# Optimization experiments

Hardware: AMD Instinct MI355X
Metric: run time of the kernel (lower is better)

Reference implementation:

```python
import jax, jax.numpy as jnp
import numpy as np

TOTAL_N = 1_048_576
FEAT = 128
B = 8
VOX_AXIS = 40  # 40**3 = 64000 <= num_vox (65535) hard-coded in the kernel
SUBBUCK = 2    # module asserts subbuck_size == 2


def setup_inputs() -> dict:
    key = jax.random.key(0)
    k1, k2 = jax.random.split(key)
    coords = jax.random.uniform(k1, (TOTAL_N, 3), dtype=jnp.float32) * 100.0
    input_feat = jax.random.normal(k2, (TOTAL_N, FEAT), dtype=jnp.float32)
    # seps = exclusive-scan ends of each batch instance (equal-size instances)
    seps = jnp.arange(1, B + 1, dtype=jnp.int32) * (TOTAL_N // B)
    return {"coords": coords, "input_feat": input_feat, "seps": seps}


def _bucket_order(coords, seps):
    """Per-instance voxel-bucket assignment + stable sort; returns (order, unpool_ind, inst_id)."""
    n = coords.shape[0]
    nb = seps.shape[0]
    # instance id of every point from cumulative boundaries
    inst_id = jnp.searchsorted(seps, jnp.arange(n, dtype=seps.dtype), side="right").astype(jnp.int32)
    # per-instance bounding box (bbox_min / bbox_max buffers in the CUDA kernel)
    bmin = jax.ops.segment_min(coords, inst_id, num_segments=nb)
    bmax = jax.ops.segment_max(coords, inst_id, num_segments=nb)
    lo, hi = bmin[inst_id], bmax[inst_id]
    u = (coords - lo) / jnp.maximum(hi - lo, jnp.float32(1e-12))
    q = jnp.clip((u * VOX_AXIS).astype(jnp.int32), 0, VOX_AXIS - 1)  # (N,3) voxel coords
    vox_id = (q[:, 0] * VOX_AXIS + q[:, 1]) * VOX_AXIS + q[:, 2]      # subbuck_id
    # stable sort by (instance, voxel) so spatially-colocated points are adjacent
    key = inst_id.astype(jnp.int64) * (VOX_AXIS ** 3) + vox_id.astype(jnp.int64)
    order = jnp.argsort(key)  # jnp.argsort is stable
    # consecutive pairs in sorted order form one subbucket of size 2
    reduced_rank = jnp.arange(n, dtype=jnp.int32) // SUBBUCK
    unpool_ind = jnp.zeros((n,), dtype=jnp.int32).at[order].set(reduced_rank)
    return order, unpool_ind, inst_id


def reference(coords, input_feat, seps):
    n = input_feat.shape[0]
    reduced_n = n // SUBBUCK
    _, unpool_ind, _ = _bucket_order(coords, seps)
    # mean reduction (reduction_op = 0 = O_MEAN) over each subbucket of 2 points
    reduced_feat = jax.ops.segment_sum(input_feat, unpool_ind, num_segments=reduced_n) / SUBBUCK
    reduced_coord = jax.ops.segment_sum(coords, unpool_ind, num_segments=reduced_n) / SUBBUCK
    reduced_sep = seps // SUBBUCK
    return reduced_coord, reduced_sep, reduced_feat, unpool_ind
```

## Files before the change

### kernel.cpp

```cpp
#include <hip/hip_runtime.h>


#define VOXA 40
#define VOX3 64000
#define SCAN_CHUNK 2048

__device__ __forceinline__ int inst_of(int i, const int* __restrict__ seps, int B) {
  int lo = 0, hi = B;
  while (lo < hi) { int m = (lo + hi) >> 1; if (seps[m] > i) hi = m; else lo = m + 1; }
  return lo;
}

__device__ __forceinline__ unsigned fmap(float f) {
  unsigned u = __float_as_uint(f);
  return (u & 0x80000000u) ? ~u : (u | 0x80000000u);
}
__device__ __forceinline__ float funmap(unsigned u) {
  unsigned b = (u & 0x80000000u) ? (u ^ 0x80000000u) : ~u;
  return __uint_as_float(b);
}

__global__ void k_init(int* hist, int* cursor, unsigned* bbox, int K, int B3) {
  int i = blockIdx.x * blockDim.x + threadIdx.x;
  if (i < K) { hist[i] = 0; cursor[i] = 0; }
  if (i < B3) { bbox[i] = 0xFFFFFFFFu; bbox[B3 + i] = 0u; }
}

__global__ void k_bbox(const float* __restrict__ coords, const int* __restrict__ seps,
                       int N, int B, unsigned* __restrict__ bbox) {
  const int CH = 1024;
  int cs = blockIdx.x * CH;
  if (cs >= N) return;
  int ce = min(cs + CH, N);
  __shared__ int uni;
  int t = threadIdx.x;
  if (t == 0) {
    int i0 = inst_of(cs, seps, B);
    int i1 = inst_of(ce - 1, seps, B);
    uni = (i0 == i1) ? i0 : -1;
  }
  __syncthreads();
  if (uni >= 0) {
    float mn0 = 3.4e38f, mn1 = 3.4e38f, mn2 = 3.4e38f;
    float mx0 = -3.4e38f, mx1 = -3.4e38f, mx2 = -3.4e38f;
    for (int i = cs + t; i < ce; i += 256) {
      float c0 = coords[i * 3 + 0], c1 = coords[i * 3 + 1], c2 = coords[i * 3 + 2];
      mn0 = fminf(mn0, c0); mn1 = fminf(mn1, c1); mn2 = fminf(mn2, c2);
      mx0 = fmaxf(mx0, c0); mx1 = fmaxf(mx1, c1); mx2 = fmaxf(mx2, c2);
    }
    __shared__ float sm[6][256];
    sm[0][t] = mn0; sm[1][t] = mn1; sm[2][t] = mn2;
    sm[3][t] = mx0; sm[4][t] = mx1; sm[5][t] = mx2;
    __syncthreads();
    for (int s = 128; s > 0; s >>= 1) {
      if (t < s) {
        sm[0][t] = fminf(sm[0][t], sm[0][t + s]);
        sm[1][t] = fminf(sm[1][t], sm[1][t + s]);
        sm[2][t] = fminf(sm[2][t], sm[2][t + s]);
        sm[3][t] = fmaxf(sm[3][t], sm[3][t + s]);
        sm[4][t] = fmaxf(sm[4][t], sm[4][t + s]);
        sm[5][t] = fmaxf(sm[5][t], sm[5][t + s]);
      }
      __syncthreads();
    }
    if (t == 0) {
      int b = uni;
      atomicMin(&bbox[b * 3 + 0], fmap(sm[0][0]));
      atomicMin(&bbox[b * 3 + 1], fmap(sm[1][0]));
      atomicMin(&bbox[b * 3 + 2], fmap(sm[2][0]));
      atomicMax(&bbox[B * 3 + b * 3 + 0], fmap(sm[3][0]));
      atomicMax(&bbox[B * 3 + b * 3 + 1], fmap(sm[4][0]));
      atomicMax(&bbox[B * 3 + b * 3 + 2], fmap(sm[5][0]));
    }
  } else {
    for (int i = cs + t; i < ce; i += 256) {
      int b = inst_of(i, seps, B);
      for (int d = 0; d < 3; ++d) {
        float c = coords[i * 3 + d];
        atomicMin(&bbox[b * 3 + d], fmap(c));
        atomicMax(&bbox[B * 3 + b * 3 + d], fmap(c));
      }
    }
  }
}

__global__ void k_key(const float* __restrict__ coords, const int* __restrict__ seps,
                      int N, int B, const unsigned* __restrict__ bbox,
                      int* __restrict__ key, int* __restrict__ hist) {
  __shared__ float lo[192], hi[192];
  int t = threadIdx.x;
  if (t < 3 * B) { lo[t] = funmap(bbox[t]); hi[t] = funmap(bbox[3 * B + t]); }
  __syncthreads();
  int i = blockIdx.x * blockDim.x + t;
  if (i >= N) return;
  int b = inst_of(i, seps, B);
  int q[3];
#pragma unroll
  for (int d = 0; d < 3; ++d) {
    float c = coords[i * 3 + d];
    float l = lo[b * 3 + d];
    float u = (c - l) / fmaxf(hi[b * 3 + d] - l, 1e-12f);
    int qi = (int)(u * 40.0f);
    q[d] = min(max(qi, 0), VOXA - 1);
  }
  int k = ((q[0] * VOXA + q[1]) * VOXA + q[2]) + b * VOX3;
  key[i] = k;
  atomicAdd(&hist[k], 1);
}

__global__ void k_scan1(int* __restrict__ hist, int* __restrict__ csums, int K) {
  __shared__ int s[256];
  int t = threadIdx.x;
  int base = blockIdx.x * SCAN_CHUNK + t * 8;
  int v[8];
  int run = 0;
#pragma unroll
  for (int j = 0; j < 8; ++j) {
    int idx = base + j;
    int x = (idx < K) ? hist[idx] : 0;
    v[j] = run;
    run += x;
  }
  s[t] = run;
  __syncthreads();
  for (int off = 1; off < 256; off <<= 1) {
    int x = (t >= off) ? s[t - off] : 0;
    __syncthreads();
    s[t] += x;
    __syncthreads();
  }
  int excl = s[t] - run;
#pragma unroll
  for (int j = 0; j < 8; ++j) {
    int idx = base + j;
    if (idx < K) hist[idx] = excl + v[j];
  }
  if (t == 255) csums[blockIdx.x] = s[255];
}

__global__ void k_scan2(int* csums, int nChunks) {
  __shared__ int s[256];
  int t = threadIdx.x;
  int carry = 0;
  for (int base = 0; base < nChunks; base += 256) {
    int idx = base + t;
    int v = (idx < nChunks) ? csums[idx] : 0;
    s[t] = v;
    __syncthreads();
    for (int off = 1; off < 256; off <<= 1) {
      int x = (t >= off) ? s[t - off] : 0;
      __syncthreads();
      s[t] += x;
      __syncthreads();
    }
    if (idx < nChunks) csums[idx] = carry + s[t] - v;
    int total = s[255];
    __syncthreads();
    carry += total;
  }
}

__global__ void k_scan3(int* __restrict__ hist, const int* __restrict__ csums, int K) {
  int i = blockIdx.x * blockDim.x + threadIdx.x;
  if (i < K) hist[i] += csums[i / SCAN_CHUNK];
}

__global__ void k_place(const int* __restrict__ key, const int* __restrict__ start,
                        int* __restrict__ cursor, int* __restrict__ order, int N) {
  int i = blockIdx.x * blockDim.x + threadIdx.x;
  if (i >= N) return;
  int k = key[i];
  int r = atomicAdd(&cursor[k], 1);
  order[start[k] + r] = i;
}

__global__ void k_fix(const int* __restrict__ start, int* __restrict__ order, int K, int N) {
  int k = blockIdx.x * blockDim.x + threadIdx.x;
  if (k >= K) return;
  int s = start[k];
  int e = (k + 1 < K) ? start[k + 1] : N;
  for (int a = s + 1; a < e; ++a) {
    int v = order[a];
    int b = a - 1;
    while (b >= s && order[b] > v) { order[b + 1] = order[b]; --b; }
    order[b + 1] = v;
  }
}

__global__ void k_out_coord(const float* __restrict__ coords, const int* __restrict__ order,
                            const int* __restrict__ seps, int RN, int B,
                            float* __restrict__ out) {
  int r = blockIdx.x * blockDim.x + threadIdx.x;
  if (r < B) out[(size_t)RN * 3 + r] = (float)(seps[r] / 2);
  if (r >= RN) return;
  int a = order[2 * r], b = order[2 * r + 1];
  out[r * 3 + 0] = (coords[a * 3 + 0] + coords[b * 3 + 0]) * 0.5f;
  out[r * 3 + 1] = (coords[a * 3 + 1] + coords[b * 3 + 1]) * 0.5f;
  out[r * 3 + 2] = (coords[a * 3 + 2] + coords[b * 3 + 2]) * 0.5f;
}

__global__ void k_out_feat(const float4* __restrict__ feat4, const int* __restrict__ order,
                           int RN, float4* __restrict__ outf) {
  int tid = blockIdx.x * blockDim.x + threadIdx.x;
  if (tid >= RN * 32) return;
  int r = tid >> 5, c = tid & 31;
  int a = order[2 * r], b = order[2 * r + 1];
  float4 va = feat4[a * 32 + c], vb = feat4[b * 32 + c];
  float4 o;
  o.x = (va.x + vb.x) * 0.5f;
  o.y = (va.y + vb.y) * 0.5f;
  o.z = (va.z + vb.z) * 0.5f;
  o.w = (va.w + vb.w) * 0.5f;
  outf[tid] = o;
}

__global__ void k_out_feat_scalar(const float* __restrict__ feat, const int* __restrict__ order,
                                  int RN, float* __restrict__ outf) {
  int tid = blockIdx.x * blockDim.x + threadIdx.x;
  if (tid >= RN * 128) return;
  int r = tid >> 7, c = tid & 127;
  int a = order[2 * r], b = order[2 * r + 1];
  outf[tid] = (feat[a * 128 + c] + feat[b * 128 + c]) * 0.5f;
}

__global__ void k_out_unpool(const int* __restrict__ order, float* __restrict__ outu, int N) {
  int p = blockIdx.x * blockDim.x + threadIdx.x;
  if (p >= N) return;
  outu[order[p]] = (float)(p >> 1);
}

extern "C" void kernel_launch(void* const* d_in, const int* in_sizes, int n_in,
                              void* d_out, int out_size, void* d_ws, size_t ws_size,
                              hipStream_t stream) {
  const float* coords = (const float*)d_in[0];
  const float* feat   = (const float*)d_in[1];
  const int*   seps   = (const int*)d_in[2];

  const int N  = in_sizes[0] / 3;
  const int B  = in_sizes[2];
  const int FE = in_sizes[1] / N;
  const int RN = N / 2;
  const int K  = B * VOX3;
  const int nChunks = (K + SCAN_CHUNK - 1) / SCAN_CHUNK;

  int* hist      = (int*)d_ws;
  int* cursor    = hist + K;
  int* csums     = cursor + K;
  unsigned* bbox = (unsigned*)(csums + ((nChunks + 255) & ~255));
  int* key       = (int*)(bbox + 6 * B);
  int* order     = key + N;

  float* out        = (float*)d_out;
  float* out_coord  = out;
  float* out_feat   = out + (size_t)RN * 3 + B;
  float* out_unpool = out_feat + (size_t)RN * FE;

  const int blk = 256;
  k_init<<<(K + blk - 1) / blk, blk, 0, stream>>>(hist, cursor, bbox, K, 3 * B);
  k_bbox<<<(N + 1023) / 1024, 256, 0, stream>>>(coords, seps, N, B, bbox);
  k_key<<<(N + blk - 1) / blk, blk, 0, stream>>>(coords, seps, N, B, bbox, key, hist);
  k_scan1<<<nChunks, 256, 0, stream>>>(hist, csums, K);
  k_scan2<<<1, 256, 0, stream>>>(csums, nChunks);
  k_scan3<<<(K + blk - 1) / blk, blk, 0, stream>>>(hist, csums, K);
  k_place<<<(N + blk - 1) / blk, blk, 0, stream>>>(key, hist, cursor, order, N);
  k_fix<<<(K + blk - 1) / blk, blk, 0, stream>>>(hist, order, K, N);
  k_out_coord<<<(RN + blk - 1) / blk, blk, 0, stream>>>(coords, order, seps, RN, B, out_coord);

  bool vec_ok = (FE % 4 == 0) && ((((size_t)RN * 3 + B) & 3) == 0) && (FE == 128);
  if (vec_ok) {
    k_out_feat<<<((RN * 32) + blk - 1) / blk, blk, 0, stream>>>(
        (const float4*)feat, order, RN, (float4*)out_feat);
  } else {
    k_out_feat_scalar<<<((RN * FE) + blk - 1) / blk, blk, 0, stream>>>(
        feat, order, RN, out_feat);
  }
  k_out_unpool<<<(N + blk - 1) / blk, blk, 0, stream>>>(order, out_unpool, N);
}
```

Measured before the change: 939.0 us.

## Fuse scan-add into placement, unpool into fix, coord into feature gather

Removes the scan3 pass by adding the chunk offset on the fly in placement and reusing the histogram as the cursor array, which drops the separate cursor buffer and its zeroing. Unpool writes and seps output move into the per-bucket sort-fix kernel. Coordinate averaging is merged into the feature gather kernel, which now uses an int2 pair load plus nontemporal vector loads and stores. Seps are cached in shared memory for the key kernel. The trade-offs are more serial per-bucket work in the fix kernel and more complex index arithmetic.

```diff
diff --git a/kernel.cpp b/kernel.cpp
--- a/kernel.cpp
+++ b/kernel.cpp
@@ -4,6 +4,8 @@
 #define VOXA 40
 #define VOX3 64000
 #define SCAN_CHUNK 2048
+
+typedef float f4 __attribute__((ext_vector_type(4)));
 
 __device__ __forceinline__ int inst_of(int i, const int* __restrict__ seps, int B) {
   int lo = 0, hi = B;
@@ -11,6 +13,12 @@
   return lo;
 }
 
+__device__ __forceinline__ int inst_of_s(int i, const int* s, int B) {
+  int lo = 0, hi = B;
+  while (lo < hi) { int m = (lo + hi) >> 1; if (s[m] > i) hi = m; else lo = m + 1; }
+  return lo;
+}
+
 __device__ __forceinline__ unsigned fmap(float f) {
   unsigned u = __float_as_uint(f);
   return (u & 0x80000000u) ? ~u : (u | 0x80000000u);
@@ -20,9 +28,9 @@
   return __uint_as_float(b);
 }
 
-__global__ void k_init(int* hist, int* cursor, unsigned* bbox, int K, int B3) {
+__global__ void k_init(int* hist, unsigned* bbox, int K, int B3) {
   int i = blockIdx.x * blockDim.x + threadIdx.x;
-  if (i < K) { hist[i] = 0; cursor[i] = 0; }
+  if (i < K) hist[i] = 0;
   if (i < B3) { bbox[i] = 0xFFFFFFFFu; bbox[B3 + i] = 0u; }
 }
 
@@ -88,12 +96,14 @@
                       int N, int B, const unsigned* __restrict__ bbox,
                       int* __restrict__ key, int* __restrict__ hist) {
   __shared__ float lo[192], hi[192];
+  __shared__ int ssep[64];
   int t = threadIdx.x;
   if (t < 3 * B) { lo[t] = funmap(bbox[t]); hi[t] = funmap(bbox[3 * B + t]); }
+  if (t < B) ssep[t] = seps[t];
   __syncthreads();
   int i = blockIdx.x * blockDim.x + t;
   if (i >= N) return;
-  int b = inst_of(i, seps, B);
+  int b = inst_of_s(i, ssep, B);
   int q[3];
 #pragma unroll
   for (int d = 0; d < 3; ++d) {
@@ -160,73 +170,65 @@
   }
 }
 
-__global__ void k_scan3(int* __restrict__ hist, const int* __restrict__ csums, int K) {
-  int i = blockIdx.x * blockDim.x + threadIdx.x;
-  if (i < K) hist[i] += csums[i / SCAN_CHUNK];
-}
-
-__global__ void k_place(const int* __restrict__ key, const int* __restrict__ start,
-                        int* __restrict__ cursor, int* __restrict__ order, int N) {
+__global__ void k_place(const int* __restrict__ key, int* __restrict__ hist,
+                        const int* __restrict__ csums, int* __restrict__ order, int N) {
   int i = blockIdx.x * blockDim.x + threadIdx.x;
   if (i >= N) return;
   int k = key[i];
-  int r = atomicAdd(&cursor[k], 1);
-  order[start[k] + r] = i;
-}
-
-__global__ void k_fix(const int* __restrict__ start, int* __restrict__ order, int K, int N) {
+  int p = atomicAdd(&hist[k], 1) + csums[k / SCAN_CHUNK];
+  order[p] = i;
+}
+
+__global__ void k_fix(const int* __restrict__ hist, const int* __restrict__ csums,
+                      int* __restrict__ order, float* __restrict__ outu,
+                      const int* __restrict__ seps, float* __restrict__ out_sep,
+                      int K, int N, int B) {
   int k = blockIdx.x * blockDim.x + threadIdx.x;
+  if (k < B) out_sep[k] = (float)(seps[k] / 2);
   if (k >= K) return;
-  int s = start[k];
-  int e = (k + 1 < K) ? start[k + 1] : N;
+  int e = hist[k] + csums[k / SCAN_CHUNK];
+  int s = (k == 0) ? 0 : (hist[k - 1] + csums[(k - 1) / SCAN_CHUNK]);
   for (int a = s + 1; a < e; ++a) {
     int v = order[a];
     int b = a - 1;
     while (b >= s && order[b] > v) { order[b + 1] = order[b]; --b; }
     order[b + 1] = v;
   }
-}
-
-__global__ void k_out_coord(const float* __restrict__ coords, const int* __restrict__ order,
-                            const int* __restrict__ seps, int RN, int B,
-                            float* __restrict__ out) {
-  int r = blockIdx.x * blockDim.x + threadIdx.x;
-  if (r < B) out[(size_t)RN * 3 + r] = (float)(seps[r] / 2);
-  if (r >= RN) return;
-  int a = order[2 * r], b = order[2 * r + 1];
-  out[r * 3 + 0] = (coords[a * 3 + 0] + coords[b * 3 + 0]) * 0.5f;
-  out[r * 3 + 1] = (coords[a * 3 + 1] + coords[b * 3 + 1]) * 0.5f;
-  out[r * 3 + 2] = (coords[a * 3 + 2] + coords[b * 3 + 2]) * 0.5f;
-}
-
-__global__ void k_out_feat(const float4* __restrict__ feat4, const int* __restrict__ order,
-                           int RN, float4* __restrict__ outf) {
+  for (int p = s; p < e; ++p) outu[order[p]] = (float)(p >> 1);
+}
+
+__global__ void k_out_fused(const f4* __restrict__ feat4, const float* __restrict__ coords,
+                            const int* __restrict__ order, int RN,
+                            float* __restrict__ out_coord, f4* __restrict__ outf) {
   int tid = blockIdx.x * blockDim.x + threadIdx.x;
   if (tid >= RN * 32) return;
   int r = tid >> 5, c = tid & 31;
+  int2 ab = ((const int2*)order)[r];
+  int a = ab.x, b = ab.y;
+  f4 va = __builtin_nontemporal_load(&feat4[(size_t)a * 32 + c]);
+  f4 vb = __builtin_nontemporal_load(&feat4[(size_t)b * 32 + c]);
+  f4 o = (va + vb) * 0.5f;
+  __builtin_nontemporal_store(o, &outf[tid]);
+  if (c == 0) {
+    out_coord[r * 3 + 0] = (coords[a * 3 + 0] + coords[b * 3 + 0]) * 0.5f;
+    out_coord[r * 3 + 1] = (coords[a * 3 + 1] + coords[b * 3 + 1]) * 0.5f;
+    out_coord[r * 3 + 2] = (coords[a * 3 + 2] + coords[b * 3 + 2]) * 0.5f;
+  }
+}
+
+__global__ void k_out_fused_scalar(const float* __restrict__ feat, const float* __restrict__ coords,
+                                   const int* __restrict__ order, int RN, int FE,
+                                   float* __restrict__ out_coord, float* __restrict__ outf) {
+  int tid = blockIdx.x * blockDim.x + threadIdx.x;
+  if (tid >= RN * FE) return;
+  int r = tid / FE, c = tid % FE;
   int a = order[2 * r], b = order[2 * r + 1];
-  float4 va = feat4[a * 32 + c], vb = feat4[b * 32 + c];
-  float4 o;
-  o.x = (va.x + vb.x) * 0.5f;
-  o.y = (va.y + vb.y) * 0.5f;
-  o.z = (va.z + vb.z) * 0.5f;
-  o.w = (va.w + vb.w) * 0.5f;
-  outf[tid] = o;
-}
-
-__global__ void k_out_feat_scalar(const float* __restrict__ feat, const int* __restrict__ order,
-                                  int RN, float* __restrict__ outf) {
-  int tid = blockIdx.x * blockDim.x + threadIdx.x;
-  if (tid >= RN * 128) return;
-  int r = tid >> 7, c = tid & 127;
-  int a = order[2 * r], b = order[2 * r + 1];
-  outf[tid] = (feat[a * 128 + c] + feat[b * 128 + c]) * 0.5f;
-}
-
-__global__ void k_out_unpool(const int* __restrict__ order, float* __restrict__ outu, int N) {
-  int p = blockIdx.x * blockDim.x + threadIdx.x;
-  if (p >= N) return;
-  outu[order[p]] = (float)(p >> 1);
+  outf[tid] = (feat[(size_t)a * FE + c] + feat[(size_t)b * FE + c]) * 0.5f;
+  if (c == 0) {
+    out_coord[r * 3 + 0] = (coords[a * 3 + 0] + coords[b * 3 + 0]) * 0.5f;
+    out_coord[r * 3 + 1] = (coords[a * 3 + 1] + coords[b * 3 + 1]) * 0.5f;
+    out_coord[r * 3 + 2] = (coords[a * 3 + 2] + coords[b * 3 + 2]) * 0.5f;
+  }
 }
 
 extern "C" void kernel_launch(void* const* d_in, const int* in_sizes, int n_in,
@@ -244,35 +246,33 @@
   const int nChunks = (K + SCAN_CHUNK - 1) / SCAN_CHUNK;
 
   int* hist      = (int*)d_ws;
-  int* cursor    = hist + K;
-  int* csums     = cursor + K;
+  int* csums     = hist + K;
   unsigned* bbox = (unsigned*)(csums + ((nChunks + 255) & ~255));
   int* key       = (int*)(bbox + 6 * B);
   int* order     = key + N;
 
   float* out        = (float*)d_out;
   float* out_coord  = out;
+  float* out_sep    = out + (size_t)RN * 3;
   float* out_feat   = out + (size_t)RN * 3 + B;
   float* out_unpool = out_feat + (size_t)RN * FE;
 
   const int blk = 256;
-  k_init<<<(K + blk - 1) / blk, blk, 0, stream>>>(hist, cursor, bbox, K, 3 * B);
+  k_init<<<(K + blk - 1) / blk, blk, 0, stream>>>(hist, bbox, K, 3 * B);
   k_bbox<<<(N + 1023) / 1024, 256, 0, stream>>>(coords, seps, N, B, bbox);
   k_key<<<(N + blk - 1) / blk, blk, 0, stream>>>(coords, seps, N, B, bbox, key, hist);
   k_scan1<<<nChunks, 256, 0, stream>>>(hist, csums, K);
   k_scan2<<<1, 256, 0, stream>>>(csums, nChunks);
-  k_scan3<<<(K + blk - 1) / blk, blk, 0, stream>>>(hist, csums, K);
-  k_place<<<(N + blk - 1) / blk, blk, 0, stream>>>(key, hist, cursor, order, N);
-  k_fix<<<(K + blk - 1) / blk, blk, 0, stream>>>(hist, order, K, N);
-  k_out_coord<<<(RN + blk - 1) / blk, blk, 0, stream>>>(coords, order, seps, RN, B, out_coord);
-
-  bool vec_ok = (FE % 4 == 0) && ((((size_t)RN * 3 + B) & 3) == 0) && (FE == 128);
+  k_place<<<(N + blk - 1) / blk, blk, 0, stream>>>(key, hist, csums, order, N);
+  k_fix<<<(K + blk - 1) / blk, blk, 0, stream>>>(hist, csums, order, out_unpool,
+                                                 seps, out_sep, K, N, B);
+
+  bool vec_ok = (FE == 128) && ((((size_t)RN * 3 + B) & 3) == 0);
   if (vec_ok) {
-    k_out_feat<<<((RN * 32) + blk - 1) / blk, blk, 0, stream>>>(
-        (const float4*)feat, order, RN, (float4*)out_feat);
+    k_out_fused<<<((RN * 32) + blk - 1) / blk, blk, 0, stream>>>(
+        (const f4*)feat, coords, order, RN, out_coord, (f4*)out_feat);
   } else {
-    k_out_feat_scalar<<<((RN * FE) + blk - 1) / blk, blk, 0, stream>>>(
-        feat, order, RN, out_feat);
-  }
-  k_out_unpool<<<(N + blk - 1) / blk, blk, 0, stream>>>(order, out_unpool, N);
-}
+    k_out_fused_scalar<<<((RN * FE) + blk - 1) / blk, blk, 0, stream>>>(
+        feat, coords, order, RN, FE, out_coord, out_feat);
+  }
+}
```

Measured after the change: 916.2 us. -2.4%, faster.
